# Optimization experiments

Hardware: AMD Instinct MI355X
Metric: run time of the kernel (lower is better)

Reference implementation:

```python
import jax, jax.numpy as jnp
import numpy as np

B, L, HID, NH = 8, 1024, 1024, 16
DH = HID // NH
EPS = 1e-12


def _linear(x, W, b):
    # torch nn.Linear: y = x @ W.T + b
    return jnp.einsum('ble,oe->blo', x, W) + b


def _attend(qx, kx, vx, mask, Wq, bq, Wk, bk, Wv, bv):
    q = _linear(qx, Wq, bq).reshape(B, -1, NH, DH)
    k = _linear(kx, Wk, bk).reshape(B, -1, NH, DH)
    v = _linear(vx, Wv, bv).reshape(B, -1, NH, DH)
    scores = jnp.einsum('bqhd,bkhd->bhqk', q, k) / np.sqrt(DH).astype(np.float32)
    scores = scores + mask  # additive mask broadcast [B,1,1,Lk]
    probs = jax.nn.softmax(scores, axis=-1)  # dropout = identity (eval mode)
    ctx = jnp.einsum('bhqk,bkhd->bqhd', probs, v)
    return ctx.reshape(B, -1, HID)


def _layernorm(x, gamma, beta):
    mu = jnp.mean(x, axis=-1, keepdims=True)
    var = jnp.mean(jnp.square(x - mu), axis=-1, keepdims=True)
    return gamma * (x - mu) * jax.lax.rsqrt(var + EPS) + beta


def setup_inputs():
    key = jax.random.key(0)
    ks = jax.random.split(key, 20)
    s = 0.02
    d = {
        'cinput_tensor': jax.random.normal(ks[0], (B, L, HID), jnp.float32),
        'qinput_tensor': jax.random.normal(ks[1], (B, L, HID), jnp.float32),
        'attention_mask': jnp.zeros((B, 1, 1, L), jnp.float32),
        'qattention_mask': jnp.zeros((B, 1, 1, L), jnp.float32),
    }
    names = ['Wq', 'Wk', 'Wv', 'Wqq', 'Wqk', 'Wqv', 'Wo']
    for i, n in enumerate(names):
        d[n] = jax.random.normal(ks[2 + i], (HID, HID), jnp.float32) * s
        d['b' + n[1:]] = jnp.zeros((HID,), jnp.float32)
    d['gamma'] = jnp.ones((HID,), jnp.float32)
    d['beta'] = jnp.zeros((HID,), jnp.float32)
    return d


def reference(cinput_tensor, qinput_tensor, attention_mask, qattention_mask,
              Wq, bq, Wk, bk, Wv, bv, Wqq, bqq, Wqk, bqk, Wqv, bqv,
              Wo, bo, gamma, beta):
    enc, dec = cinput_tensor, qinput_tensor
    # c-branch: query from dec, key/value from enc
    ctx = _attend(dec, enc, enc, attention_mask, Wq, bq, Wk, bk, Wv, bv)
    # q-branch: query from enc, key/value from dec
    qctx = _attend(enc, dec, dec, qattention_mask, Wqq, bqq, Wqk, bqk, Wqv, bqv)
    # output: same dense/LayerNorm reused, and BOTH residuals add cinput_tensor
    # (faithful to the original module, including its apparent bug)
    c_out = _layernorm(_linear(ctx, Wo, bo) + cinput_tensor, gamma, beta)
    q_out = _layernorm(_linear(qctx, Wo, bo) + cinput_tensor, gamma, beta)
    return (c_out, q_out)
```

## Files before the change

kernel.cpp:

```cpp
#include <hip/hip_runtime.h>

typedef __bf16 bf16;
typedef unsigned short u16;
typedef __bf16 bf16x8 __attribute__((ext_vector_type(8)));
typedef __bf16 bf16x4 __attribute__((ext_vector_type(4)));
typedef float f32x4 __attribute__((ext_vector_type(4)));

#define GLD16(g, l) __builtin_amdgcn_global_load_lds( \
    (const __attribute__((address_space(1))) void*)(g), \
    (__attribute__((address_space(3))) void*)(l), 16, 0, 0)

#define MFMA_BF16 __builtin_amdgcn_mfma_f32_16x16x32_bf16

struct CvtSeg { const float* s; bf16* d; int n; };
struct CvtArgs { CvtSeg seg[9]; };

__global__ __launch_bounds__(256) void cvt_kernel(CvtArgs a) {
  const CvtSeg sg = a.seg[blockIdx.z];
  const int i = (blockIdx.x * 256 + threadIdx.x) * 4;
  if (i >= sg.n) return;
  const f32x4 v = *(const f32x4*)(sg.s + i);
  bf16x4 o;
  #pragma unroll
  for (int j = 0; j < 4; ++j) o[j] = (bf16)v[j];
  *(bf16x4*)(sg.d + i) = o;
}

struct GemmDesc {
  const bf16* X;
  const bf16* W;
  const float* B;
  const float* R;
  bf16* Y;
  float* Yf;
  int vt;
};
struct GemmArgs { GemmDesc d[3]; };

__global__ __launch_bounds__(256, 2) void gemm128(GemmArgs args) {
  const GemmDesc g = args.d[blockIdx.z];
  __shared__ u16 As[128 * 64];
  __shared__ u16 Bs[128 * 64];
  const int tid = threadIdx.x;
  const int w = tid >> 6, lane = tid & 63;
  const int lq = lane >> 4, ll = lane & 15;
  const int m0 = blockIdx.y * 128, n0 = blockIdx.x * 128;
  const int wm = (w >> 1) * 64, wn = (w & 1) * 64;
  f32x4 acc[4][4] = {};

  for (int k0 = 0; k0 < 1024; k0 += 64) {
    #pragma unroll
    for (int i = 0; i < 4; ++i) {
      const int sb = w * 256 + i * 64;
      const int s = sb + lane;
      const int r = s >> 3, c = (s & 7) ^ (r & 7);
      GLD16(g.X + (m0 + r) * 1024 + k0 + c * 8, &As[sb * 8]);
      GLD16(g.W + (n0 + r) * 1024 + k0 + c * 8, &Bs[sb * 8]);
    }
    __syncthreads();
    #pragma unroll
    for (int kk = 0; kk < 64; kk += 32) {
      const int cb = (kk >> 3) + lq;
      bf16x8 a[4], b[4];
      #pragma unroll
      for (int t = 0; t < 4; ++t) {
        const int m = wm + t * 16 + ll;
        a[t] = *(const bf16x8*)&As[m * 64 + ((cb ^ (m & 7)) << 3)];
        const int n = wn + t * 16 + ll;
        b[t] = *(const bf16x8*)&Bs[n * 64 + ((cb ^ (n & 7)) << 3)];
      }
      #pragma unroll
      for (int mt = 0; mt < 4; ++mt)
        #pragma unroll
        for (int nt = 0; nt < 4; ++nt)
          acc[mt][nt] = MFMA_BF16(a[mt], b[nt], acc[mt][nt], 0, 0, 0);
    }
    __syncthreads();
  }

  float biasv[4];
  #pragma unroll
  for (int nt = 0; nt < 4; ++nt) biasv[nt] = g.B[n0 + wn + nt * 16 + ll];

  #pragma unroll
  for (int mt = 0; mt < 4; ++mt) {
    #pragma unroll
    for (int r = 0; r < 4; ++r) {
      const int m = m0 + wm + mt * 16 + lq * 4 + r;
      #pragma unroll
      for (int nt = 0; nt < 4; ++nt) {
        const int n = n0 + wn + nt * 16 + ll;
        float v = acc[mt][nt][r] + biasv[nt];
        if (g.R) v += g.R[m * 1024 + n];
        if (g.Yf) {
          g.Yf[m * 1024 + n] = v;
        } else if (!g.vt) {
          g.Y[m * 1024 + n] = (bf16)v;
        } else {
          const int bb = m >> 10, tok = m & 1023;
          g.Y[(((bb << 4) + (n >> 6)) * 64 + (n & 63)) * 1024 + tok] = (bf16)v;
        }
      }
    }
  }
}

struct AttnDesc { const bf16* Qp; const bf16* Kp; const bf16* Vt; const float* mask; bf16* ctx; };

__global__ __launch_bounds__(256, 4) void attn_kernel(AttnDesc A) {
  __shared__ u16 Ks[128 * 64];
  __shared__ u16 Vts[64 * 128];
  __shared__ u16 Pts[4 * 1024];
  const int tid = threadIdx.x;
  const int w = tid >> 6, lane = tid & 63;
  const int lq = lane >> 4, ll = lane & 15;
  const int bh = blockIdx.y, b = bh >> 4, h = bh & 15;
  const int q0 = blockIdx.x * 128;
  const float* mrow = A.mask + b * 1024;

  #pragma unroll
  for (int i = 0; i < 4; ++i) {
    const int sb = w * 256 + i * 64;
    const int s = sb + lane;
    const int r = s >> 3, c = (s & 7) ^ (r & 7);
    GLD16(A.Qp + (b * 1024 + q0 + r) * 1024 + h * 64 + c * 8, &Ks[sb * 8]);
  }
  __syncthreads();
  bf16x8 bq[2][2];
  #pragma unroll
  for (int nt = 0; nt < 2; ++nt)
    #pragma unroll
    for (int kd = 0; kd < 2; ++kd) {
      const int row = w * 32 + nt * 16 + ll;
      const int c8 = kd * 4 + lq;
      bq[nt][kd] = *(const bf16x8*)&Ks[row * 64 + ((c8 ^ (row & 7)) << 3)];
    }
  __syncthreads();

  f32x4 oacc[4][2] = {};
  float rsum[2] = {0.f, 0.f};

  for (int kt = 0; kt < 8; ++kt) {
    const int kk0 = kt * 128;
    #pragma unroll
    for (int i = 0; i < 4; ++i) {
      const int sb = w * 256 + i * 64;
      const int s = sb + lane;
      { const int r = s >> 3, c = (s & 7) ^ (r & 7);
        GLD16(A.Kp + (b * 1024 + kk0 + r) * 1024 + h * 64 + c * 8, &Ks[sb * 8]); }
      { const int r = s >> 4, c = (s & 15) ^ (r & 15);
        GLD16(A.Vt + (bh * 64 + r) * 1024 + kk0 + c * 8, &Vts[sb * 8]); }
    }
    __syncthreads();

    #pragma unroll
    for (int qtr = 0; qtr < 4; ++qtr) {
      bf16x8 ak[2][2];
      #pragma unroll
      for (int mh = 0; mh < 2; ++mh) {
        const int row = qtr * 32 + mh * 16 + ll;
        #pragma unroll
        for (int kd = 0; kd < 2; ++kd) {
          const int c8 = kd * 4 + lq;
          ak[mh][kd] = *(const bf16x8*)&Ks[row * 64 + ((c8 ^ (row & 7)) << 3)];
        }
      }
      f32x4 sacc[2][2] = {};
      #pragma unroll
      for (int mh = 0; mh < 2; ++mh)
        #pragma unroll
        for (int nt = 0; nt < 2; ++nt)
          #pragma unroll
          for (int kd = 0; kd < 2; ++kd)
            sacc[mh][nt] = MFMA_BF16(ak[mh][kd], bq[nt][kd], sacc[mh][nt], 0, 0, 0);

      f32x4 mv[2];
      #pragma unroll
      for (int mh = 0; mh < 2; ++mh)
        mv[mh] = *(const f32x4*)&mrow[kk0 + qtr * 32 + mh * 16 + lq * 4];

      #pragma unroll
      for (int mh = 0; mh < 2; ++mh)
        #pragma unroll
        for (int nt = 0; nt < 2; ++nt) {
          bf16x4 pv;
          #pragma unroll
          for (int rr = 0; rr < 4; ++rr) {
            const float p = __expf(fmaf(sacc[mh][nt][rr], 0.125f, mv[mh][rr]));
            rsum[nt] += p;
            pv[rr] = (bf16)p;
          }
          const int row = nt * 16 + ll;
          const int g = mh * 2 + (lq >> 1);
          *(bf16x4*)&Pts[w * 1024 + row * 32 + ((g ^ (row & 3)) << 3) + (lq & 1) * 4] = pv;
        }

      bf16x8 bp[2];
      #pragma unroll
      for (int nt = 0; nt < 2; ++nt) {
        const int row = nt * 16 + ll;
        bp[nt] = *(const bf16x8*)&Pts[w * 1024 + row * 32 + ((lq ^ (row & 3)) << 3)];
      }
      #pragma unroll
      for (int mtd = 0; mtd < 4; ++mtd) {
        const int row = mtd * 16 + ll;
        const int c16 = (qtr * 4 + lq) ^ (row & 15);
        const bf16x8 av = *(const bf16x8*)&Vts[row * 128 + (c16 << 3)];
        oacc[mtd][0] = MFMA_BF16(av, bp[0], oacc[mtd][0], 0, 0, 0);
        oacc[mtd][1] = MFMA_BF16(av, bp[1], oacc[mtd][1], 0, 0, 0);
      }
    }
    __syncthreads();
  }

  #pragma unroll
  for (int nt = 0; nt < 2; ++nt) {
    rsum[nt] += __shfl_xor(rsum[nt], 16, 64);
    rsum[nt] += __shfl_xor(rsum[nt], 32, 64);
  }

  #pragma unroll
  for (int nt = 0; nt < 2; ++nt) {
    const float inv = 1.f / rsum[nt];
    const int tok = q0 + w * 32 + nt * 16 + ll;
    #pragma unroll
    for (int mtd = 0; mtd < 4; ++mtd) {
      bf16x4 ov;
      #pragma unroll
      for (int rr = 0; rr < 4; ++rr) ov[rr] = (bf16)(oacc[mtd][nt][rr] * inv);
      *(bf16x4*)&A.ctx[(size_t)(b * 1024 + tok) * 1024 + h * 64 + mtd * 16 + lq * 4] = ov;
    }
  }
}

__global__ __launch_bounds__(256) void ln_kernel(float* __restrict__ io,
                                                 const float* __restrict__ gamma,
                                                 const float* __restrict__ beta) {
  const int row = blockIdx.x;
  float* p = io + (size_t)row * 1024;
  const int t = threadIdx.x;
  const f32x4 xv = *(const f32x4*)(p + t * 4);
  float s = 0.f, ss = 0.f;
  #pragma unroll
  for (int i = 0; i < 4; ++i) { s += xv[i]; ss += xv[i] * xv[i]; }
  #pragma unroll
  for (int off = 1; off < 64; off <<= 1) { s += __shfl_xor(s, off, 64); ss += __shfl_xor(ss, off, 64); }
  __shared__ float red[8];
  const int w = t >> 6, lane = t & 63;
  if (lane == 0) { red[w * 2] = s; red[w * 2 + 1] = ss; }
  __syncthreads();
  s  = red[0] + red[2] + red[4] + red[6];
  ss = red[1] + red[3] + red[5] + red[7];
  const float mu = s * (1.f / 1024.f);
  float var = ss * (1.f / 1024.f) - mu * mu;
  var = fmaxf(var, 0.f);
  const float rs = rsqrtf(var + 1e-12f);
  const f32x4 gv = *(const f32x4*)(gamma + t * 4);
  const f32x4 bv = *(const f32x4*)(beta + t * 4);
  f32x4 yv;
  #pragma unroll
  for (int i = 0; i < 4; ++i) yv[i] = gv[i] * (xv[i] - mu) * rs + bv[i];
  *(f32x4*)(p + t * 4) = yv;
}

extern "C" void kernel_launch(void* const* d_in, const int* in_sizes, int n_in,
                              void* d_out, int out_size, void* d_ws, size_t ws_size,
                              hipStream_t stream) {
  const float* enc    = (const float*)d_in[0];
  const float* dec    = (const float*)d_in[1];
  const float* mask_c = (const float*)d_in[2];
  const float* mask_q = (const float*)d_in[3];
  const float* Wq  = (const float*)d_in[4];  const float* bq  = (const float*)d_in[5];
  const float* Wk  = (const float*)d_in[6];  const float* bk  = (const float*)d_in[7];
  const float* Wv  = (const float*)d_in[8];  const float* bv  = (const float*)d_in[9];
  const float* Wqq = (const float*)d_in[10]; const float* bqq = (const float*)d_in[11];
  const float* Wqk = (const float*)d_in[12]; const float* bqk = (const float*)d_in[13];
  const float* Wqv = (const float*)d_in[14]; const float* bqv = (const float*)d_in[15];
  const float* Wo  = (const float*)d_in[16]; const float* bo  = (const float*)d_in[17];
  const float* gamma = (const float*)d_in[18];
  const float* beta  = (const float*)d_in[19];
  float* out = (float*)d_out;

  bf16* ws = (bf16*)d_ws;
  const size_t XSZ = (size_t)8192 * 1024;
  const size_t WSZ = (size_t)1024 * 1024;
  bf16* enc_b = ws;
  bf16* dec_b = enc_b + XSZ;
  bf16* Wb[7];
  for (int i = 0; i < 7; ++i) Wb[i] = dec_b + XSZ + i * WSZ;
  bf16* Q   = Wb[6] + WSZ;
  bf16* K   = Q + XSZ;
  bf16* Vt  = K + XSZ;
  bf16* ctx_c = Vt + XSZ;
  bf16* ctx_q = ctx_c + XSZ;

  CvtArgs ca;
  ca.seg[0] = {enc, enc_b, (int)XSZ};
  ca.seg[1] = {dec, dec_b, (int)XSZ};
  const float* Wsrc[7] = {Wq, Wk, Wv, Wqq, Wqk, Wqv, Wo};
  for (int i = 0; i < 7; ++i) ca.seg[2 + i] = {Wsrc[i], Wb[i], (int)WSZ};
  cvt_kernel<<<dim3(8192, 1, 9), 256, 0, stream>>>(ca);

  GemmArgs pa;
  pa.d[0] = {dec_b, Wb[0], bq, nullptr, Q,  nullptr, 0};
  pa.d[1] = {enc_b, Wb[1], bk, nullptr, K,  nullptr, 0};
  pa.d[2] = {enc_b, Wb[2], bv, nullptr, Vt, nullptr, 1};
  gemm128<<<dim3(8, 64, 3), 256, 0, stream>>>(pa);

  AttnDesc a0 = {Q, K, Vt, mask_c, ctx_c};
  attn_kernel<<<dim3(8, 128), 256, 0, stream>>>(a0);

  GemmArgs pb;
  pb.d[0] = {enc_b, Wb[3], bqq, nullptr, Q,  nullptr, 0};
  pb.d[1] = {dec_b, Wb[4], bqk, nullptr, K,  nullptr, 0};
  pb.d[2] = {dec_b, Wb[5], bqv, nullptr, Vt, nullptr, 1};
  gemm128<<<dim3(8, 64, 3), 256, 0, stream>>>(pb);

  AttnDesc a1 = {Q, K, Vt, mask_q, ctx_q};
  attn_kernel<<<dim3(8, 128), 256, 0, stream>>>(a1);

  GemmArgs oa = {};
  oa.d[0] = {ctx_c, Wb[6], bo, enc, nullptr, out,       0};
  oa.d[1] = {ctx_q, Wb[6], bo, enc, nullptr, out + XSZ, 0};
  gemm128<<<dim3(8, 64, 2), 256, 0, stream>>>(oa);

  ln_kernel<<<dim3(16384), 256, 0, stream>>>(out, gamma, beta);
}
```

Measured before the change: 542.1 us.

## Batch both attention branches into single launches and store pre-LayerNorm in bf16

Merges the two branches' QKV projections into one 6-way GEMM launch and the two attention passes into one launch with a z-dimension selector, when the workspace is large enough. The output projection now writes its pre-LayerNorm sum as bf16 into reused buffers, and LayerNorm reads bf16 and writes fp32 to the output, which cuts the fp32 round trip. The convert kernel uses a flat grid with segment offsets, so blocks no longer sit idle on the short weight segments. The cost is more workspace and extra rounding, since the pre-LayerNorm residual sum is now quantised to bf16.

Measured after the change: 516.1 us. 1.05x faster.

```diff
diff --git a/kernel.cpp b/kernel.cpp
--- a/kernel.cpp
+++ b/kernel.cpp
@@ -12,18 +12,19 @@
 
 #define MFMA_BF16 __builtin_amdgcn_mfma_f32_16x16x32_bf16
 
-struct CvtSeg { const float* s; bf16* d; int n; };
-struct CvtArgs { CvtSeg seg[9]; };
-
-__global__ __launch_bounds__(256) void cvt_kernel(CvtArgs a) {
-  const CvtSeg sg = a.seg[blockIdx.z];
-  const int i = (blockIdx.x * 256 + threadIdx.x) * 4;
-  if (i >= sg.n) return;
-  const f32x4 v = *(const f32x4*)(sg.s + i);
+struct CvtFlat { const float* s[9]; bf16* d[9]; int off[10]; };
+
+__global__ __launch_bounds__(256) void cvt_flat(CvtFlat a) {
+  const int g = blockIdx.x * 256 + threadIdx.x;
+  int seg = 0;
+  #pragma unroll
+  for (int i = 1; i < 9; ++i) seg += (g >= a.off[i]) ? 1 : 0;
+  const int loc = (g - a.off[seg]) * 4;
+  const f32x4 v = *(const f32x4*)(a.s[seg] + loc);
   bf16x4 o;
   #pragma unroll
   for (int j = 0; j < 4; ++j) o[j] = (bf16)v[j];
-  *(bf16x4*)(sg.d + i) = o;
+  *(bf16x4*)(a.d[seg] + loc) = o;
 }
 
 struct GemmDesc {
@@ -32,10 +33,9 @@
   const float* B;
   const float* R;
   bf16* Y;
-  float* Yf;
   int vt;
 };
-struct GemmArgs { GemmDesc d[3]; };
+struct GemmArgs { GemmDesc d[6]; };
 
 __global__ __launch_bounds__(256, 2) void gemm128(GemmArgs args) {
   const GemmDesc g = args.d[blockIdx.z];
@@ -92,9 +92,7 @@
         const int n = n0 + wn + nt * 16 + ll;
         float v = acc[mt][nt][r] + biasv[nt];
         if (g.R) v += g.R[m * 1024 + n];
-        if (g.Yf) {
-          g.Yf[m * 1024 + n] = v;
-        } else if (!g.vt) {
+        if (!g.vt) {
           g.Y[m * 1024 + n] = (bf16)v;
         } else {
           const int bb = m >> 10, tok = m & 1023;
@@ -107,7 +105,8 @@
 
 struct AttnDesc { const bf16* Qp; const bf16* Kp; const bf16* Vt; const float* mask; bf16* ctx; };
 
-__global__ __launch_bounds__(256, 4) void attn_kernel(AttnDesc A) {
+__global__ __launch_bounds__(256, 4) void attn_kernel(AttnDesc A0, AttnDesc A1) {
+  const AttnDesc A = blockIdx.z ? A1 : A0;
   __shared__ u16 Ks[128 * 64];
   __shared__ u16 Vts[64 * 128];
   __shared__ u16 Pts[4 * 1024];
@@ -191,8 +190,8 @@
             pv[rr] = (bf16)p;
           }
           const int row = nt * 16 + ll;
-          const int g = mh * 2 + (lq >> 1);
-          *(bf16x4*)&Pts[w * 1024 + row * 32 + ((g ^ (row & 3)) << 3) + (lq & 1) * 4] = pv;
+          const int gq = mh * 2 + (lq >> 1);
+          *(bf16x4*)&Pts[w * 1024 + row * 32 + ((gq ^ (row & 3)) << 3) + (lq & 1) * 4] = pv;
         }
 
       bf16x8 bp[2];
@@ -233,16 +232,20 @@
   }
 }
 
-__global__ __launch_bounds__(256) void ln_kernel(float* __restrict__ io,
+__global__ __launch_bounds__(256) void ln_kernel(const bf16* __restrict__ pre_c,
+                                                 const bf16* __restrict__ pre_q,
                                                  const float* __restrict__ gamma,
-                                                 const float* __restrict__ beta) {
+                                                 const float* __restrict__ beta,
+                                                 float* __restrict__ out) {
   const int row = blockIdx.x;
-  float* p = io + (size_t)row * 1024;
+  const bf16* src = (row < 8192) ? (pre_c + (size_t)row * 1024)
+                                 : (pre_q + (size_t)(row - 8192) * 1024);
+  float* dst = out + (size_t)row * 1024;
   const int t = threadIdx.x;
-  const f32x4 xv = *(const f32x4*)(p + t * 4);
-  float s = 0.f, ss = 0.f;
-  #pragma unroll
-  for (int i = 0; i < 4; ++i) { s += xv[i]; ss += xv[i] * xv[i]; }
+  const bf16x4 xv = *(const bf16x4*)(src + t * 4);
+  float x[4]; float s = 0.f, ss = 0.f;
+  #pragma unroll
+  for (int i = 0; i < 4; ++i) { x[i] = (float)xv[i]; s += x[i]; ss += x[i] * x[i]; }
   #pragma unroll
   for (int off = 1; off < 64; off <<= 1) { s += __shfl_xor(s, off, 64); ss += __shfl_xor(ss, off, 64); }
   __shared__ float red[8];
@@ -259,8 +262,8 @@
   const f32x4 bv = *(const f32x4*)(beta + t * 4);
   f32x4 yv;
   #pragma unroll
-  for (int i = 0; i < 4; ++i) yv[i] = gv[i] * (xv[i] - mu) * rs + bv[i];
-  *(f32x4*)(p + t * 4) = yv;
+  for (int i = 0; i < 4; ++i) yv[i] = gv[i] * (x[i] - mu) * rs + bv[i];
+  *(f32x4*)(dst + t * 4) = yv;
 }
 
 extern "C" void kernel_launch(void* const* d_in, const int* in_sizes, int n_in,
@@ -288,41 +291,81 @@
   bf16* dec_b = enc_b + XSZ;
   bf16* Wb[7];
   for (int i = 0; i < 7; ++i) Wb[i] = dec_b + XSZ + i * WSZ;
-  bf16* Q   = Wb[6] + WSZ;
-  bf16* K   = Q + XSZ;
-  bf16* Vt  = K + XSZ;
-  bf16* ctx_c = Vt + XSZ;
-  bf16* ctx_q = ctx_c + XSZ;
-
-  CvtArgs ca;
-  ca.seg[0] = {enc, enc_b, (int)XSZ};
-  ca.seg[1] = {dec, dec_b, (int)XSZ};
+  bf16* after_w = Wb[6] + WSZ;
+
+  CvtFlat ca;
+  ca.s[0] = enc; ca.d[0] = enc_b;
+  ca.s[1] = dec; ca.d[1] = dec_b;
   const float* Wsrc[7] = {Wq, Wk, Wv, Wqq, Wqk, Wqv, Wo};
-  for (int i = 0; i < 7; ++i) ca.seg[2 + i] = {Wsrc[i], Wb[i], (int)WSZ};
-  cvt_kernel<<<dim3(8192, 1, 9), 256, 0, stream>>>(ca);
-
-  GemmArgs pa;
-  pa.d[0] = {dec_b, Wb[0], bq, nullptr, Q,  nullptr, 0};
-  pa.d[1] = {enc_b, Wb[1], bk, nullptr, K,  nullptr, 0};
-  pa.d[2] = {enc_b, Wb[2], bv, nullptr, Vt, nullptr, 1};
-  gemm128<<<dim3(8, 64, 3), 256, 0, stream>>>(pa);
-
-  AttnDesc a0 = {Q, K, Vt, mask_c, ctx_c};
-  attn_kernel<<<dim3(8, 128), 256, 0, stream>>>(a0);
-
-  GemmArgs pb;
-  pb.d[0] = {enc_b, Wb[3], bqq, nullptr, Q,  nullptr, 0};
-  pb.d[1] = {dec_b, Wb[4], bqk, nullptr, K,  nullptr, 0};
-  pb.d[2] = {dec_b, Wb[5], bqv, nullptr, Vt, nullptr, 1};
-  gemm128<<<dim3(8, 64, 3), 256, 0, stream>>>(pb);
-
-  AttnDesc a1 = {Q, K, Vt, mask_q, ctx_q};
-  attn_kernel<<<dim3(8, 128), 256, 0, stream>>>(a1);
-
-  GemmArgs oa = {};
-  oa.d[0] = {ctx_c, Wb[6], bo, enc, nullptr, out,       0};
-  oa.d[1] = {ctx_q, Wb[6], bo, enc, nullptr, out + XSZ, 0};
-  gemm128<<<dim3(8, 64, 2), 256, 0, stream>>>(oa);
-
-  ln_kernel<<<dim3(16384), 256, 0, stream>>>(out, gamma, beta);
-}
+  for (int i = 0; i < 7; ++i) { ca.s[2 + i] = Wsrc[i]; ca.d[2 + i] = Wb[i]; }
+  int running = 0;
+  const int segn[9] = {(int)(XSZ / 4), (int)(XSZ / 4), (int)(WSZ / 4), (int)(WSZ / 4),
+                       (int)(WSZ / 4), (int)(WSZ / 4), (int)(WSZ / 4), (int)(WSZ / 4), (int)(WSZ / 4)};
+  for (int i = 0; i < 9; ++i) { ca.off[i] = running; running += segn[i]; }
+  ca.off[9] = running;
+  const int cvt_blocks = running / 256;
+
+  const size_t need_par = (size_t)(23 + 48) * 1024 * 1024 * 2;
+
+  cvt_flat<<<dim3(cvt_blocks), 256, 0, stream>>>(ca);
+
+  if (ws_size >= need_par) {
+    bf16* Qc  = after_w;        bf16* Kc  = Qc + XSZ;  bf16* Vtc = Kc + XSZ;
+    bf16* Qq  = Vtc + XSZ;      bf16* Kq  = Qq + XSZ;  bf16* Vtq = Kq + XSZ;
+    bf16* ctx_c = enc_b;
+    bf16* ctx_q = dec_b;
+    bf16* pre_c = Qc;
+    bf16* pre_q = Qq;
+
+    GemmArgs pa = {};
+    pa.d[0] = {dec_b, Wb[0], bq,  nullptr, Qc,  0};
+    pa.d[1] = {enc_b, Wb[1], bk,  nullptr, Kc,  0};
+    pa.d[2] = {enc_b, Wb[2], bv,  nullptr, Vtc, 1};
+    pa.d[3] = {enc_b, Wb[3], bqq, nullptr, Qq,  0};
+    pa.d[4] = {dec_b, Wb[4], bqk, nullptr, Kq,  0};
+    pa.d[5] = {dec_b, Wb[5], bqv, nullptr, Vtq, 1};
+    gemm128<<<dim3(8, 64, 6), 256, 0, stream>>>(pa);
+
+    AttnDesc a0 = {Qc, Kc, Vtc, mask_c, ctx_c};
+    AttnDesc a1 = {Qq, Kq, Vtq, mask_q, ctx_q};
+    attn_kernel<<<dim3(8, 128, 2), 256, 0, stream>>>(a0, a1);
+
+    GemmArgs oa = {};
+    oa.d[0] = {ctx_c, Wb[6], bo, enc, pre_c, 0};
+    oa.d[1] = {ctx_q, Wb[6], bo, enc, pre_q, 0};
+    gemm128<<<dim3(8, 64, 2), 256, 0, stream>>>(oa);
+
+    ln_kernel<<<dim3(16384), 256, 0, stream>>>(pre_c, pre_q, gamma, beta, out);
+  } else {
+    bf16* Q  = after_w;  bf16* K = Q + XSZ;  bf16* Vt = K + XSZ;
+    bf16* ctx_c = Vt + XSZ;
+    bf16* ctx_q = ctx_c + XSZ;
+    bf16* pre_c = Q;
+    bf16* pre_q = K;
+
+    GemmArgs pa = {};
+    pa.d[0] = {dec_b, Wb[0], bq,  nullptr, Q,  0};
+    pa.d[1] = {enc_b, Wb[1], bk,  nullptr, K,  0};
+    pa.d[2] = {enc_b, Wb[2], bv,  nullptr, Vt, 1};
+    gemm128<<<dim3(8, 64, 3), 256, 0, stream>>>(pa);
+
+    AttnDesc a0 = {Q, K, Vt, mask_c, ctx_c};
+    attn_kernel<<<dim3(8, 128, 1), 256, 0, stream>>>(a0, a0);
+
+    GemmArgs pb = {};
+    pb.d[0] = {enc_b, Wb[3], bqq, nullptr, Q,  0};
+    pb.d[1] = {dec_b, Wb[4], bqk, nullptr, K,  0};
+    pb.d[2] = {dec_b, Wb[5], bqv, nullptr, Vt, 1};
+    gemm128<<<dim3(8, 64, 3), 256, 0, stream>>>(pb);
+
+    AttnDesc a1 = {Q, K, Vt, mask_q, ctx_q};
+    attn_kernel<<<dim3(8, 128, 1), 256, 0, stream>>>(a1, a1);
+
+    GemmArgs oa = {};
+    oa.d[0] = {ctx_c, Wb[6], bo, enc, pre_c, 0};
+    oa.d[1] = {ctx_q, Wb[6], bo, enc, pre_q, 0};
+    gemm128<<<dim3(8, 64, 2), 256, 0, stream>>>(oa);
+
+    ln_kernel<<<dim3(16384), 256, 0, stream>>>(pre_c, pre_q, gamma, beta, out);
+  }
+}
```
